# Kernel optimization log

Measured on AMD Instinct MI355X. Metric: run time of the kernel, lower is better.

The kernel has to match this reference:

```python
import jax, jax.numpy as jnp
import numpy as np

N = 10000
E = 160000
B = 16
NEG_SLOPE = 0.2


def gat_conv(x, src, dst, W, a_src, a_dst, b, heads, ch):
    # x: [N, F_in]; src/dst: [E'] (self-loops included); W: [F_in, heads*ch]
    n = x.shape[0]
    h = (x @ W).reshape(n, heads, ch)                     # [N,H,C]
    alpha_src = jnp.sum(h * a_src, axis=-1)               # [N,H]
    alpha_dst = jnp.sum(h * a_dst, axis=-1)               # [N,H]
    e = jax.nn.leaky_relu(alpha_src[src] + alpha_dst[dst], NEG_SLOPE)  # [E,H]
    # segment softmax over edges grouped by destination node
    m = jax.ops.segment_max(e, dst, num_segments=n)       # [N,H]
    ex = jnp.exp(e - m[dst])                              # [E,H]
    denom = jax.ops.segment_sum(ex, dst, num_segments=n)  # [N,H]
    alpha = ex / denom[dst]                               # [E,H]
    out = jax.ops.segment_sum(alpha[:, :, None] * h[src], dst, num_segments=n)  # [N,H,C]
    return out.reshape(n, heads * ch) + b


def setup_inputs() -> dict:
    key = jax.random.key(0)
    ks = jax.random.split(key, 16)
    glorot = lambda k, shp: jax.random.normal(k, shp, jnp.float32) * np.sqrt(2.0 / (shp[0] + shp[-1]))
    inp = {
        "x": jax.random.normal(ks[0], (N, 128), jnp.float32),
        "edge_index": jax.random.randint(ks[1], (2, E), 0, N, jnp.int64),
        "batch": jnp.sort(jax.random.randint(ks[2], (N,), 0, B, jnp.int64)),
        # conv1: 128 -> 128 per head, 8 heads
        "W1": glorot(ks[3], (128, 8 * 128)),
        "att_src1": glorot(ks[4], (8, 128)),
        "att_dst1": glorot(ks[5], (8, 128)),
        "b1": jnp.zeros((8 * 128,), jnp.float32),
        # conv2: 1024 -> 64 per head, 8 heads
        "W2": glorot(ks[6], (1024, 8 * 64)),
        "att_src2": glorot(ks[7], (8, 64)),
        "att_dst2": glorot(ks[8], (8, 64)),
        "b2": jnp.zeros((8 * 64,), jnp.float32),
        "fc1_w": glorot(ks[9], (512, 32)),
        "fc1_b": jnp.zeros((32,), jnp.float32),
        "fc2_w": glorot(ks[10], (32, 10)),
        "fc2_b": jnp.zeros((10,), jnp.float32),
    }
    return inp


def reference(x, edge_index, batch, W1, att_src1, att_dst1, b1,
              W2, att_src2, att_dst2, b2, fc1_w, fc1_b, fc2_w, fc2_b):
    n = x.shape[0]
    loop = jnp.arange(n, dtype=edge_index.dtype)
    src = jnp.concatenate([edge_index[0], loop])  # PyG add_self_loops=True
    dst = jnp.concatenate([edge_index[1], loop])
    h = jax.nn.elu(gat_conv(x, src, dst, W1, att_src1, att_dst1, b1, 8, 128))   # [N,1024]
    h = jax.nn.elu(gat_conv(h, src, dst, W2, att_src2, att_dst2, b2, 8, 64))    # [N,512]
    # global mean pool over graphs
    sums = jax.ops.segment_sum(h, batch, num_segments=B)                        # [B,512]
    cnt = jax.ops.segment_sum(jnp.ones((n,), h.dtype), batch, num_segments=B)
    g = sums / jnp.maximum(cnt, 1.0)[:, None]
    g = jax.nn.elu(g @ fc1_w + fc1_b)
    return g @ fc2_w + fc2_b                                                    # [B,10]
```

## Files before the change

### kernel.cpp

```cpp
#include <hip/hip_runtime.h>
#include <math.h>

#define HEADS 8
#define NEG 0.2f

typedef unsigned short ushort_t;
typedef __attribute__((ext_vector_type(8))) short short8;
typedef float f32x4 __attribute__((ext_vector_type(4)));

__device__ inline ushort_t f2bf(float f) {
  union { float f; unsigned u; } v; v.f = f;
  unsigned r = (v.u + 0x7FFF + ((v.u >> 16) & 1)) >> 16;
  return (ushort_t)r;
}

__device__ inline float4 bf4(uint2 v) {
  union { unsigned u; float f; } a, b, c, d;
  a.u = v.x << 16; b.u = v.x & 0xffff0000u;
  c.u = v.y << 16; d.u = v.y & 0xffff0000u;
  return make_float4(a.f, b.f, c.f, d.f);
}

__device__ inline float elu_f(float v) {
  return (v > 0.f) ? v : (__expf(v) - 1.f);
}

__global__ __launch_bounds__(256) void init_k(int* __restrict__ ws, int zero_words,
                                              const float* __restrict__ x,
                                              ushort_t* __restrict__ xb,
                                              const float* __restrict__ W1,
                                              ushort_t* __restrict__ w1t,
                                              const float* __restrict__ W2,
                                              ushort_t* __restrict__ w2t, int nx4) {
  __shared__ float tile[32][33];
  int blk = blockIdx.x;
  if (blk < 640) {
    const float* W; ushort_t* Wt; int K, N, tk, tn;
    if (blk < 128) { W = W1; Wt = w1t; K = 128; N = 1024; tk = blk >> 5; tn = blk & 31; }
    else { W = W2; Wt = w2t; K = 1024; N = 512; int t = blk - 128; tk = t >> 4; tn = t & 15; }
    int tx = threadIdx.x & 31, ty = threadIdx.x >> 5;
    int k0 = tk * 32, n0 = tn * 32;
#pragma unroll
    for (int r = 0; r < 4; r++)
      tile[ty + r * 8][tx] = W[(size_t)(k0 + ty + r * 8) * N + n0 + tx];
    __syncthreads();
#pragma unroll
    for (int r = 0; r < 4; r++)
      Wt[(size_t)(n0 + ty + r * 8) * K + k0 + tx] = f2bf(tile[tx][ty + r * 8]);
  } else {
    int i = (blk - 640) * 256 + threadIdx.x;
    if (i < zero_words) ws[i] = 0;
    if (i < nx4) {
      float4 v = ((const float4*)x)[i];
      ushort_t o[4] = {f2bf(v.x), f2bf(v.y), f2bf(v.z), f2bf(v.w)};
      *(uint2*)&xb[i * 4] = *(uint2*)o;
    }
  }
}

__global__ void prep_k(const int* __restrict__ ei, int* __restrict__ src,
                       int* __restrict__ dst, int* __restrict__ deg,
                       const int* __restrict__ batch, int* __restrict__ bstart,
                       int* __restrict__ bend, int E, int Nn) {
  int i = blockIdx.x * blockDim.x + threadIdx.x;
  if (i < Nn) {
    int b = batch[i];
    if (i == 0 || batch[i - 1] != b) bstart[b] = i;
    if (i == Nn - 1 || batch[i + 1] != b) bend[b] = i + 1;
  }
  if (i >= E + Nn) return;
  int s, d;
  if (i < E) { s = ei[i]; d = ei[E + i]; }
  else       { s = d = i - E; }
  src[i] = s;
  dst[i] = d;
  atomicAdd(&deg[d], 1);
}

__global__ __launch_bounds__(1024) void scan_k(const int* __restrict__ deg,
                                               int* __restrict__ offs,
                                               int* __restrict__ cursor, int Nn) {
  __shared__ int wtot[16];
  __shared__ int wexcl[16];
  __shared__ int soff_s;
  int t = threadIdx.x;
  int lane = t & 63, w = t >> 6;
  if (t == 0) soff_s = 0;
  __syncthreads();
  for (int base = 0; base < Nn; base += 4096) {
    int idx = base + 4 * t;
    int4 v = make_int4(0, 0, 0, 0);
    if (idx + 3 < Nn) v = *(const int4*)&deg[idx];
    else {
      if (idx < Nn)     v.x = deg[idx];
      if (idx + 1 < Nn) v.y = deg[idx + 1];
      if (idx + 2 < Nn) v.z = deg[idx + 2];
      if (idx + 3 < Nn) v.w = deg[idx + 3];
    }
    int s1 = v.x, s2 = s1 + v.y, s3 = s2 + v.z, s4 = s3 + v.w;
    int sc = s4;
#pragma unroll
    for (int o = 1; o < 64; o <<= 1) {
      int x = __shfl_up(sc, o);
      if (lane >= o) sc += x;
    }
    if (lane == 63) wtot[w] = sc;
    __syncthreads();
    if (w == 0) {
      int tv = (lane < 16) ? wtot[lane] : 0;
      int ts = tv;
#pragma unroll
      for (int o = 1; o < 16; o <<= 1) {
        int x = __shfl_up(ts, o);
        if (lane >= o) ts += x;
      }
      if (lane < 16) wexcl[lane] = ts - tv;
      if (lane == 15) wtot[15] = ts;
    }
    __syncthreads();
    int excl = soff_s + wexcl[w] + (sc - s4);
    int o0 = excl, o1 = excl + s1, o2 = excl + s2, o3 = excl + s3;
    if (idx < Nn)     { offs[idx] = o0;     cursor[idx] = o0; }
    if (idx + 1 < Nn) { offs[idx + 1] = o1; cursor[idx + 1] = o1; }
    if (idx + 2 < Nn) { offs[idx + 2] = o2; cursor[idx + 2] = o2; }
    if (idx + 3 < Nn) { offs[idx + 3] = o3; cursor[idx + 3] = o3; }
    int chunk_total = wtot[15];
    __syncthreads();
    if (t == 0) soff_s += chunk_total;
    __syncthreads();
  }
  if (t == 0) offs[Nn] = soff_s;
}

__global__ void scatter_k(const int* __restrict__ src, const int* __restrict__ dst,
                          int* __restrict__ cursor, int* __restrict__ psrc, int Etot) {
  int i = blockIdx.x * blockDim.x + threadIdx.x;
  if (i >= Etot) return;
  int p = atomicAdd(&cursor[dst[i]], 1);
  psrc[p] = src[i];
}

#define LDA 72
__global__ __launch_bounds__(256) void mfma_gemm_k(const ushort_t* __restrict__ A,
                                                   const ushort_t* __restrict__ Bt,
                                                   ushort_t* __restrict__ Cb,
                                                   const float* __restrict__ att_s,
                                                   const float* __restrict__ att_d,
                                                   float* __restrict__ asrc,
                                                   float* __restrict__ adst,
                                                   int M, int N, int K, int CSHIFT) {
  __shared__ ushort_t As[128 * LDA];
  __shared__ ushort_t Bs[128 * LDA];
  int tid = threadIdx.x;
  int lane = tid & 63;
  int wave = tid >> 6;
  int wm = (wave >> 1) * 64, wn = (wave & 1) * 64;
  int bm = blockIdx.y * 128, bn = blockIdx.x * 128;
  int lrow = lane & 15, lq = lane >> 4;

  f32x4 acc[4][4];
#pragma unroll
  for (int i = 0; i < 4; i++)
#pragma unroll
    for (int j = 0; j < 4; j++) acc[i][j] = 0.f;

  int srow = tid >> 2;
  int skc = (tid & 3) * 8;

  int gr0 = min(bm + srow, M - 1);
  int gr1 = min(bm + srow + 64, M - 1);
  const ushort_t* pa0 = &A[(size_t)gr0 * K + skc];
  const ushort_t* pa1 = &A[(size_t)gr1 * K + skc];
  const ushort_t* pb0 = &Bt[(size_t)(bn + srow) * K + skc];
  const ushort_t* pb1 = &Bt[(size_t)(bn + srow + 64) * K + skc];

  short8 va0 = *(const short8*)pa0;
  short8 va1 = *(const short8*)(pa0 + 32);
  short8 va2 = *(const short8*)pa1;
  short8 va3 = *(const short8*)(pa1 + 32);
  short8 vb0 = *(const short8*)pb0;
  short8 vb1 = *(const short8*)(pb0 + 32);
  short8 vb2 = *(const short8*)pb1;
  short8 vb3 = *(const short8*)(pb1 + 32);

  for (int k0 = 0; k0 < K; k0 += 64) {
    __syncthreads();
    *(short8*)&As[srow * LDA + skc] = va0;
    *(short8*)&As[srow * LDA + 32 + skc] = va1;
    *(short8*)&As[(srow + 64) * LDA + skc] = va2;
    *(short8*)&As[(srow + 64) * LDA + 32 + skc] = va3;
    *(short8*)&Bs[srow * LDA + skc] = vb0;
    *(short8*)&Bs[srow * LDA + 32 + skc] = vb1;
    *(short8*)&Bs[(srow + 64) * LDA + skc] = vb2;
    *(short8*)&Bs[(srow + 64) * LDA + 32 + skc] = vb3;
    __syncthreads();
    if (k0 + 64 < K) {
      int kn = k0 + 64;
      va0 = *(const short8*)(pa0 + kn);
      va1 = *(const short8*)(pa0 + kn + 32);
      va2 = *(const short8*)(pa1 + kn);
      va3 = *(const short8*)(pa1 + kn + 32);
      vb0 = *(const short8*)(pb0 + kn);
      vb1 = *(const short8*)(pb0 + kn + 32);
      vb2 = *(const short8*)(pb1 + kn);
      vb3 = *(const short8*)(pb1 + kn + 32);
    }
#pragma unroll
    for (int ks = 0; ks < 2; ks++) {
      short8 af[4], bfr[4];
#pragma unroll
      for (int t = 0; t < 4; t++) {
        af[t]  = *(const short8*)&As[(wm + t * 16 + lrow) * LDA + ks * 32 + lq * 8];
        bfr[t] = *(const short8*)&Bs[(wn + t * 16 + lrow) * LDA + ks * 32 + lq * 8];
      }
#pragma unroll
      for (int i = 0; i < 4; i++)
#pragma unroll
        for (int j = 0; j < 4; j++)
          acc[i][j] = __builtin_amdgcn_mfma_f32_16x16x32_bf16(af[i], bfr[j], acc[i][j], 0, 0, 0);
    }
  }

  {
    int hh = (bn + wn) >> CSHIFT;
    float avs[4], avd[4];
#pragma unroll
    for (int j = 0; j < 4; j++) {
      int col = bn + wn + j * 16 + lrow;
      avs[j] = att_s[col];
      avd[j] = att_d[col];
    }
#pragma unroll
    for (int i = 0; i < 4; i++) {
#pragma unroll
      for (int r = 0; r < 4; r++) {
        float ps = 0.f, pd = 0.f;
#pragma unroll
        for (int j = 0; j < 4; j++) {
          float v = acc[i][j][r];
          ps += v * avs[j];
          pd += v * avd[j];
        }
#pragma unroll
        for (int o = 1; o < 16; o <<= 1) {
          ps += __shfl_xor(ps, o);
          pd += __shfl_xor(pd, o);
        }
        int row = bm + wm + i * 16 + lq * 4 + r;
        if (lrow == 0 && row < M) {
          atomicAdd(&asrc[row * HEADS + hh], ps);
          atomicAdd(&adst[row * HEADS + hh], pd);
        }
      }
    }
  }

#pragma unroll
  for (int i = 0; i < 4; i++) {
    int row0 = bm + wm + i * 16 + lq * 4;
#pragma unroll
    for (int j = 0; j < 4; j++) {
      int col = bn + wn + j * 16 + lrow;
#pragma unroll
      for (int r = 0; r < 4; r++) {
        int row = row0 + r;
        if (row < M) Cb[(size_t)row * N + col] = f2bf(acc[i][j][r]);
      }
    }
  }
}

template <int F, int CSHIFT, int BT, int NSPLIT, typename OT>
__global__ __launch_bounds__(BT) void aggregate_k(const ushort_t* __restrict__ hb,
                                                  const float* __restrict__ asrc,
                                                  const float* __restrict__ adst,
                                                  const int* __restrict__ offs,
                                                  const int* __restrict__ psrc,
                                                  const float* __restrict__ bias,
                                                  OT* __restrict__ out) {
  constexpr int CPB = F / NSPLIT;
  static_assert(CPB == 4 * BT, "CPB/thread mismatch");
  int nb = blockIdx.x;
  int n = nb / NSPLIT;
  int coff = (nb - n * NSPLIT) * CPB;
  int t = threadIdx.x;
  int c0 = coff + 4 * t;
  int hh = c0 >> CSHIFT;
  float adn = adst[n * HEADS + hh];
  int e0 = offs[n], e1 = offs[n + 1];
  float4 acc = make_float4(0.f, 0.f, 0.f, 0.f);
  float wsum = 0.f;

  int i = e0;
  int s[8];
  if (i + 8 <= e1) {
#pragma unroll
    for (int u = 0; u < 8; u++) s[u] = psrc[i + u];
  }
  while (i + 8 <= e1) {
    uint2 r[8];
    float av[8];
#pragma unroll
    for (int u = 0; u < 8; u++) r[u] = *(const uint2*)&hb[(size_t)s[u] * F + c0];
#pragma unroll
    for (int u = 0; u < 8; u++) av[u] = asrc[s[u] * HEADS + hh];
    i += 8;
    bool more = (i + 8 <= e1);
    int sn[8];
#pragma unroll
    for (int u = 0; u < 8; u++) sn[u] = more ? psrc[i + u] : 0;
#pragma unroll
    for (int u = 0; u < 8; u++) {
      float v = av[u] + adn;
      v = (v > 0.f) ? v : NEG * v;
      float w = __expf(v);
      float4 f = bf4(r[u]);
      wsum += w;
      acc.x += w * f.x;
      acc.y += w * f.y;
      acc.z += w * f.z;
      acc.w += w * f.w;
    }
#pragma unroll
    for (int u = 0; u < 8; u++) s[u] = sn[u];
  }
  for (; i < e1; i++) {
    int ss = psrc[i];
    float v = asrc[ss * HEADS + hh] + adn;
    v = (v > 0.f) ? v : NEG * v;
    float w = __expf(v);
    float4 f = bf4(*(const uint2*)&hb[(size_t)ss * F + c0]);
    wsum += w;
    acc.x += w * f.x; acc.y += w * f.y;
    acc.z += w * f.z; acc.w += w * f.w;
  }

  float inv = 1.f / wsum;
  float v0 = elu_f(acc.x * inv + bias[c0]);
  float v1 = elu_f(acc.y * inv + bias[c0 + 1]);
  float v2 = elu_f(acc.z * inv + bias[c0 + 2]);
  float v3 = elu_f(acc.w * inv + bias[c0 + 3]);
  if (sizeof(OT) == 2) {
    unsigned p0 = (unsigned)f2bf(v0) | ((unsigned)f2bf(v1) << 16);
    unsigned p1 = (unsigned)f2bf(v2) | ((unsigned)f2bf(v3) << 16);
    *(uint2*)&((ushort_t*)out)[(size_t)n * F + c0] = make_uint2(p0, p1);
  } else {
    *(float4*)&((float*)out)[(size_t)n * F + c0] = make_float4(v0, v1, v2, v3);
  }
}

__global__ __launch_bounds__(256) void pool_k(const float* __restrict__ g,
                                              const int* __restrict__ batch,
                                              float* __restrict__ sums, int Nn) {
  int c = blockIdx.x * 256 + threadIdx.x;
  int n0 = blockIdx.y * 50;
  int n1 = min(n0 + 50, Nn);
  if (n0 >= n1) return;
  float acc = 0.f;
  int cur = batch[n0];
  for (int n = n0; n < n1; n++) {
    int b = batch[n];
    if (b != cur) { atomicAdd(&sums[cur * 512 + c], acc); acc = 0.f; cur = b; }
    acc += g[(size_t)n * 512 + c];
  }
  atomicAdd(&sums[cur * 512 + c], acc);
}

__global__ __launch_bounds__(512) void mlp_k(const float* __restrict__ sums,
                                             const int* __restrict__ bstart,
                                             const int* __restrict__ bend,
                                             const float* __restrict__ w1,
                                             const float* __restrict__ b1,
                                             const float* __restrict__ w2,
                                             const float* __restrict__ b2,
                                             float* __restrict__ out) {
  __shared__ float gm[16 * 512];
  __shared__ float t1[16 * 32];
  int t = threadIdx.x;
  for (int i = t; i < 16 * 512; i += 512) {
    int b = i >> 9;
    float c = (float)(bend[b] - bstart[b]);
    gm[i] = sums[i] / fmaxf(c, 1.f);
  }
  __syncthreads();
  {
    int b = t >> 5, j = t & 31;
    float s = b1[j];
    for (int k = 0; k < 512; k++) s += gm[(b << 9) + k] * w1[k * 32 + j];
    t1[t] = elu_f(s);
  }
  __syncthreads();
  if (t < 160) {
    int b = t / 10, j = t - b * 10;
    float s = b2[j];
#pragma unroll
    for (int k = 0; k < 32; k++) s += t1[b * 32 + k] * w2[k * 10 + j];
    out[t] = s;
  }
}

extern "C" void kernel_launch(void* const* d_in, const int* in_sizes, int n_in,
                              void* d_out, int out_size, void* d_ws, size_t ws_size,
                              hipStream_t stream) {
  const float* x   = (const float*)d_in[0];
  const int*   ei  = (const int*)d_in[1];
  const int* batch = (const int*)d_in[2];
  const float* W1  = (const float*)d_in[3];
  const float* as1 = (const float*)d_in[4];
  const float* ad1 = (const float*)d_in[5];
  const float* b1  = (const float*)d_in[6];
  const float* W2  = (const float*)d_in[7];
  const float* as2 = (const float*)d_in[8];
  const float* ad2 = (const float*)d_in[9];
  const float* b2  = (const float*)d_in[10];
  const float* f1w = (const float*)d_in[11];
  const float* f1b = (const float*)d_in[12];
  const float* f2w = (const float*)d_in[13];
  const float* f2b = (const float*)d_in[14];
  float* out = (float*)d_out;

  const int Nn = in_sizes[2];
  const int E = in_sizes[1] / 2;
  const int Etot = E + Nn;

  size_t off = 0;
  auto alloc = [&](size_t elems) { size_t o = off; off += (elems + 63) & ~(size_t)63; return o; };
  int* wsi = (int*)d_ws;
  float* wsf = (float*)d_ws;

  size_t o_deg  = alloc(Nn);
  size_t o_pool = alloc(16 * 512);
  size_t o_as1  = alloc((size_t)Nn * 8);
  size_t o_ad1  = alloc((size_t)Nn * 8);
  size_t o_as2  = alloc((size_t)Nn * 8);
  size_t o_ad2  = alloc((size_t)Nn * 8);
  size_t zero_words = off;
  size_t o_bst  = alloc(64);
  size_t o_ben  = alloc(64);
  size_t o_offs = alloc(Nn + 1);
  size_t o_cur  = alloc(Nn);
  size_t o_src  = alloc(Etot);
  size_t o_dst  = alloc(Etot);
  size_t o_psrc = alloc(Etot);
  size_t o_xb   = alloc((size_t)Nn * 128 / 2);
  size_t o_w1t  = alloc(1024 * 128 / 2);
  size_t o_w2t  = alloc(512 * 1024 / 2);
  size_t o_h    = alloc((size_t)Nn * 1024 / 2);
  size_t o_g    = alloc((size_t)Nn * 1024);

  ushort_t* xb  = (ushort_t*)(wsi + o_xb);
  ushort_t* w1t = (ushort_t*)(wsi + o_w1t);
  ushort_t* w2t = (ushort_t*)(wsi + o_w2t);
  ushort_t* hb  = (ushort_t*)(wsi + o_h);
  ushort_t* g1b = (ushort_t*)(wsi + o_g);

  int eb = (Etot + 255) / 256;

  int nx4 = Nn * 128 / 4;
  int ep_work = (int)((zero_words > (size_t)nx4 ? zero_words : (size_t)nx4));
  int init_blocks = 640 + (ep_work + 255) / 256;
  init_k<<<init_blocks, 256, 0, stream>>>(wsi, (int)zero_words, x, xb,
                                          W1, w1t, W2, w2t, nx4);
  prep_k<<<eb, 256, 0, stream>>>(ei, wsi + o_src, wsi + o_dst, wsi + o_deg,
                                 batch, wsi + o_bst, wsi + o_ben, E, Nn);
  scan_k<<<1, 1024, 0, stream>>>(wsi + o_deg, wsi + o_offs, wsi + o_cur, Nn);
  scatter_k<<<eb, 256, 0, stream>>>(wsi + o_src, wsi + o_dst, wsi + o_cur,
                                    wsi + o_psrc, Etot);

  mfma_gemm_k<<<dim3(1024 / 128, (Nn + 127) / 128), 256, 0, stream>>>(
      xb, w1t, hb, as1, ad1, wsf + o_as1, wsf + o_ad1, Nn, 1024, 128, 7);
  aggregate_k<1024, 7, 128, 2, ushort_t><<<Nn * 2, 128, 0, stream>>>(
      hb, wsf + o_as1, wsf + o_ad1, wsi + o_offs, wsi + o_psrc, b1, g1b);

  mfma_gemm_k<<<dim3(512 / 128, (Nn + 127) / 128), 256, 0, stream>>>(
      g1b, w2t, hb, as2, ad2, wsf + o_as2, wsf + o_ad2, Nn, 512, 1024, 6);
  aggregate_k<512, 6, 64, 2, float><<<Nn * 2, 64, 0, stream>>>(
      hb, wsf + o_as2, wsf + o_ad2, wsi + o_offs, wsi + o_psrc, b2, wsf + o_g);

  pool_k<<<dim3(2, (Nn + 49) / 50), 256, 0, stream>>>(wsf + o_g, batch, wsf + o_pool, Nn);
  mlp_k<<<1, 512, 0, stream>>>(wsf + o_pool, wsi + o_bst, wsi + o_ben, f1w, f1b, f2w, f2b, out);
}
```

Measured before the change: 274.9 us.

## Load GEMM tiles directly into LDS with global_load_lds and XOR swizzle

Replaces the register-staged global-to-LDS tile copy in the MFMA GEMM with direct global_load_lds 16-byte transfers, and swaps the padded LDS layout for an XOR-swizzled unpadded layout to avoid bank conflicts. This saves VGPRs and the LDS store instructions. It also drops the register prefetch of the next tile, so global loads are no longer overlapped with the MFMA work of the previous tile within a block. There is no explicit vmcnt wait before the barrier, so correctness depends on the compiler inserting one.

```diff
diff --git a/kernel.cpp b/kernel.cpp
--- a/kernel.cpp
+++ b/kernel.cpp
@@ -24,6 +24,11 @@
 __device__ inline float elu_f(float v) {
   return (v > 0.f) ? v : (__expf(v) - 1.f);
 }
+
+#define GLDS16(gp, lp)                                                          \
+  __builtin_amdgcn_global_load_lds(                                             \
+      (const __attribute__((address_space(1))) void*)(gp),                      \
+      (__attribute__((address_space(3))) void*)(lp), 16, 0, 0)
 
 __global__ __launch_bounds__(256) void init_k(int* __restrict__ ws, int zero_words,
                                               const float* __restrict__ x,
@@ -140,7 +145,6 @@
   psrc[p] = src[i];
 }
 
-#define LDA 72
 __global__ __launch_bounds__(256) void mfma_gemm_k(const ushort_t* __restrict__ A,
                                                    const ushort_t* __restrict__ Bt,
                                                    ushort_t* __restrict__ Cb,
@@ -149,8 +153,8 @@
                                                    float* __restrict__ asrc,
                                                    float* __restrict__ adst,
                                                    int M, int N, int K, int CSHIFT) {
-  __shared__ ushort_t As[128 * LDA];
-  __shared__ ushort_t Bs[128 * LDA];
+  __shared__ __attribute__((aligned(16))) ushort_t As[128 * 64];
+  __shared__ __attribute__((aligned(16))) ushort_t Bs[128 * 64];
   int tid = threadIdx.x;
   int lane = tid & 63;
   int wave = tid >> 6;
@@ -164,54 +168,37 @@
 #pragma unroll
     for (int j = 0; j < 4; j++) acc[i][j] = 0.f;
 
-  int srow = tid >> 2;
-  int skc = (tid & 3) * 8;
-
-  int gr0 = min(bm + srow, M - 1);
-  int gr1 = min(bm + srow + 64, M - 1);
-  const ushort_t* pa0 = &A[(size_t)gr0 * K + skc];
-  const ushort_t* pa1 = &A[(size_t)gr1 * K + skc];
-  const ushort_t* pb0 = &Bt[(size_t)(bn + srow) * K + skc];
-  const ushort_t* pb1 = &Bt[(size_t)(bn + srow + 64) * K + skc];
-
-  short8 va0 = *(const short8*)pa0;
-  short8 va1 = *(const short8*)(pa0 + 32);
-  short8 va2 = *(const short8*)pa1;
-  short8 va3 = *(const short8*)(pa1 + 32);
-  short8 vb0 = *(const short8*)pb0;
-  short8 vb1 = *(const short8*)(pb0 + 32);
-  short8 vb2 = *(const short8*)pb1;
-  short8 vb3 = *(const short8*)(pb1 + 32);
+  int srow = lane >> 3;
+  int scol = 8 * ((lane & 7) ^ srow);
+  const ushort_t* pa[4];
+  const ushort_t* pb[4];
+  ushort_t* la[4];
+  ushort_t* lb[4];
+#pragma unroll
+  for (int c = 0; c < 4; c++) {
+    int row = wave * 32 + c * 8 + srow;
+    int ga = min(bm + row, M - 1);
+    pa[c] = &A[(size_t)ga * K + scol];
+    pb[c] = &Bt[(size_t)(bn + row) * K + scol];
+    la[c] = &As[(wave * 4 + c) * 512];
+    lb[c] = &Bs[(wave * 4 + c) * 512];
+  }
 
   for (int k0 = 0; k0 < K; k0 += 64) {
     __syncthreads();
-    *(short8*)&As[srow * LDA + skc] = va0;
-    *(short8*)&As[srow * LDA + 32 + skc] = va1;
-    *(short8*)&As[(srow + 64) * LDA + skc] = va2;
-    *(short8*)&As[(srow + 64) * LDA + 32 + skc] = va3;
-    *(short8*)&Bs[srow * LDA + skc] = vb0;
-    *(short8*)&Bs[srow * LDA + 32 + skc] = vb1;
-    *(short8*)&Bs[(srow + 64) * LDA + skc] = vb2;
-    *(short8*)&Bs[(srow + 64) * LDA + 32 + skc] = vb3;
-    __syncthreads();
-    if (k0 + 64 < K) {
-      int kn = k0 + 64;
-      va0 = *(const short8*)(pa0 + kn);
-      va1 = *(const short8*)(pa0 + kn + 32);
-      va2 = *(const short8*)(pa1 + kn);
-      va3 = *(const short8*)(pa1 + kn + 32);
-      vb0 = *(const short8*)(pb0 + kn);
-      vb1 = *(const short8*)(pb0 + kn + 32);
-      vb2 = *(const short8*)(pb1 + kn);
-      vb3 = *(const short8*)(pb1 + kn + 32);
-    }
+#pragma unroll
+    for (int c = 0; c < 4; c++) GLDS16(pa[c] + k0, la[c]);
+#pragma unroll
+    for (int c = 0; c < 4; c++) GLDS16(pb[c] + k0, lb[c]);
+    __syncthreads();
 #pragma unroll
     for (int ks = 0; ks < 2; ks++) {
       short8 af[4], bfr[4];
 #pragma unroll
       for (int t = 0; t < 4; t++) {
-        af[t]  = *(const short8*)&As[(wm + t * 16 + lrow) * LDA + ks * 32 + lq * 8];
-        bfr[t] = *(const short8*)&Bs[(wn + t * 16 + lrow) * LDA + ks * 32 + lq * 8];
+        int cbs = (ks * 64 + lq * 16) ^ ((lrow & 7) << 4);
+        af[t]  = *(const short8*)&As[(wm + t * 16 + lrow) * 64 + (cbs >> 1)];
+        bfr[t] = *(const short8*)&Bs[(wn + t * 16 + lrow) * 64 + (cbs >> 1)];
       }
 #pragma unroll
       for (int i = 0; i < 4; i++)
```

New measurement: 276.4 us. No clear change (+0.5%).
